# Kernel optimization log

Hardware: AMD Instinct MI355X
Metric: run time of the kernel (lower is better)

The kernel has to match this reference:

```python
import jax, jax.numpy as jnp
import numpy as np

NUM_RANGES = 256
DOPPLER = 64
EMBED = 16
MAX_ELE = 37
MAX_AZI = 107
K_PER_RANGE = 512
IN_DIM = DOPPLER + 2 * EMBED  # 96


def setup_inputs() -> dict:
    key = jax.random.key(0)
    ks = jax.random.split(key, 12)
    N = NUM_RANGES * K_PER_RANGE
    s = 1.0 / np.sqrt(IN_DIM)  # torch Linear default init scale
    return {
        "power_vals": jax.random.normal(ks[0], (N, DOPPLER), dtype=jnp.float32),
        "ele_indices": jax.random.randint(ks[1], (N,), 0, MAX_ELE, dtype=jnp.int32),
        "range_indices": jax.random.randint(ks[2], (N,), 0, NUM_RANGES, dtype=jnp.int32),
        "azi_indices": jax.random.randint(ks[3], (N,), 0, MAX_AZI, dtype=jnp.int32),
        "ele_table": jax.random.normal(ks[4], (MAX_ELE, EMBED), dtype=jnp.float32),
        "azi_table": jax.random.normal(ks[5], (MAX_AZI, EMBED), dtype=jnp.float32),
        "Wq": jax.random.uniform(ks[6], (DOPPLER, IN_DIM), jnp.float32, -s, s),
        "bq": jax.random.uniform(ks[7], (DOPPLER,), jnp.float32, -s, s),
        "Wk": jax.random.uniform(ks[8], (DOPPLER, IN_DIM), jnp.float32, -s, s),
        "bk": jax.random.uniform(ks[9], (DOPPLER,), jnp.float32, -s, s),
        "Wv": jax.random.uniform(ks[10], (DOPPLER, IN_DIM), jnp.float32, -s, s),
        "bv": jax.random.uniform(ks[11], (DOPPLER,), jnp.float32, -s, s),
    }


def reference(power_vals, ele_indices, range_indices, azi_indices,
              ele_table, azi_table, Wq, bq, Wk, bk, Wv, bv):
    Kp = power_vals.shape[0] // NUM_RANGES
    # embedding gather + concat: [R, K, D + 2E]
    ele_e = ele_table[ele_indices.reshape(NUM_RANGES, Kp)]
    azi_e = azi_table[azi_indices.reshape(NUM_RANGES, Kp)]
    pv = power_vals.reshape(NUM_RANGES, Kp, DOPPLER)
    x = jnp.concatenate([pv, ele_e, azi_e], axis=-1)
    # QKV projections (torch Linear: x @ W.T + b)
    Q = jnp.einsum('rkf,df->rkd', x, Wq) + bq
    Kt = jnp.einsum('rkf,df->rkd', x, Wk) + bk
    V = jnp.einsum('rkf,df->rkd', x, Wv) + bv
    scores = jnp.einsum('rqd,rkd->rqk', Q, Kt) / jnp.sqrt(jnp.float32(DOPPLER))
    attn = jax.nn.softmax(scores, axis=-1)
    attended = jnp.einsum('rqk,rkd->rqd', attn, V)
    attended_sum = attended.sum(axis=-1)  # [R, K]
    return attended_sum.reshape(-1)
```

## Files before the change

### kernel.cpp

```cpp
#include <hip/hip_runtime.h>


#define SCALE 0.18033688011112042f

typedef __bf16 bf16;
typedef bf16 v4bf __attribute__((ext_vector_type(4)));
typedef bf16 v8bf __attribute__((ext_vector_type(8)));
typedef float v4f __attribute__((ext_vector_type(4)));

__device__ __forceinline__ v8bf pk8(float4 a, float4 b) {
    v8bf r;
    r[0] = (bf16)a.x; r[1] = (bf16)a.y; r[2] = (bf16)a.z; r[3] = (bf16)a.w;
    r[4] = (bf16)b.x; r[5] = (bf16)b.y; r[6] = (bf16)b.z; r[7] = (bf16)b.w;
    return r;
}
__device__ __forceinline__ float d4(float4 a, v4f w) {
    return a.x * w[0] + a.y * w[1] + a.z * w[2] + a.w * w[3];
}

__global__ __launch_bounds__(1024, 4)
void sda_kernel(const float* __restrict__ power,
                const int*   __restrict__ ele_i,
                const int*   __restrict__ azi_i,
                const float* __restrict__ ele_t,
                const float* __restrict__ azi_t,
                const float* __restrict__ Wq, const float* __restrict__ bq,
                const float* __restrict__ Wk, const float* __restrict__ bk,
                const float* __restrict__ Wv, const float* __restrict__ bv,
                float* __restrict__ out)
{
    extern __shared__ char smem[];
    char*  Kb   = smem;
    float* vsum = (float*)(smem + 65536);
    float* wvs  = (float*)(smem + 67584);

    const int tid  = threadIdx.x;
    const int wave = tid >> 6;
    const int lane = tid & 63;
    const int l15  = lane & 15;
    const int quad = lane >> 4;
    const int rowbase = blockIdx.x * 512 + wave * 32;

    if (tid < 96) {
        float s = 0.f;
#pragma unroll 8
        for (int r = 0; r < 64; r++) s += Wv[r * 96 + tid];
        wvs[tid] = s;
    } else if (tid == 96) {
        float s = 0.f;
#pragma unroll
        for (int d = 0; d < 64; d++) s += bv[d];
        wvs[96] = s;
    }
    __syncthreads();

    v4f w0 = *(const v4f*)(wvs + quad * 8);
    v4f w1 = *(const v4f*)(wvs + quad * 8 + 4);
    v4f w2 = *(const v4f*)(wvs + 32 + quad * 8);
    v4f w3 = *(const v4f*)(wvs + 32 + quad * 8 + 4);
    v4f w4 = *(const v4f*)(wvs + 64 + quad * 8);
    v4f w5 = *(const v4f*)(wvs + 64 + quad * 8 + 4);
    const float bvs = wvs[96];

    v8bf xa[2][3];
#pragma unroll
    for (int mt = 0; mt < 2; mt++) {
        int row = rowbase + mt * 16 + l15;
        const float* pr = power + (size_t)row * 64;
        float4 a0 = *(const float4*)(pr + quad * 8);
        float4 a1 = *(const float4*)(pr + quad * 8 + 4);
        float4 a2 = *(const float4*)(pr + 32 + quad * 8);
        float4 a3 = *(const float4*)(pr + 32 + quad * 8 + 4);
        int ie = ele_i[row];
        int ia = azi_i[row];
        const float* tb = (quad < 2) ? (ele_t + ie * 16 + quad * 8)
                                     : (azi_t + ia * 16 + (quad - 2) * 8);
        float4 a4 = *(const float4*)tb;
        float4 a5 = *(const float4*)(tb + 4);
        xa[mt][0] = pk8(a0, a1);
        xa[mt][1] = pk8(a2, a3);
        xa[mt][2] = pk8(a4, a5);
        float d = d4(a0, w0) + d4(a1, w1) + d4(a2, w2) + d4(a3, w3) + d4(a4, w4) + d4(a5, w5);
        d += __shfl_xor(d, 16);
        d += __shfl_xor(d, 32);
        if (quad == 0) vsum[wave * 32 + mt * 16 + l15] = d + bvs;
    }

    char* Sw = Kb + wave * 4096;
#pragma unroll
    for (int mtd = 0; mtd < 4; mtd++) {
        v8bf wq3[3];
#pragma unroll
        for (int kt = 0; kt < 3; kt++) {
            const float* p = Wq + (mtd * 16 + l15) * 96 + kt * 32 + quad * 8;
            wq3[kt] = pk8(*(const float4*)p, *(const float4*)(p + 4));
        }
        float4 bq4 = *(const float4*)(bq + mtd * 16 + quad * 4);
#pragma unroll
        for (int ntr = 0; ntr < 2; ntr++) {
            v4f acc = {0.f, 0.f, 0.f, 0.f};
#pragma unroll
            for (int kt = 0; kt < 3; kt++)
                acc = __builtin_amdgcn_mfma_f32_16x16x32_bf16(wq3[kt], xa[ntr][kt], acc, 0, 0, 0);
            int row = ntr * 16 + l15;
            v4bf o;
            o[0] = (bf16)((acc[0] + bq4.x) * SCALE);
            o[1] = (bf16)((acc[1] + bq4.y) * SCALE);
            o[2] = (bf16)((acc[2] + bq4.z) * SCALE);
            o[3] = (bf16)((acc[3] + bq4.w) * SCALE);
            *(v4bf*)(Sw + row * 128 +
                     ((((mtd * 2 + (quad >> 1)) ^ (row & 7)) << 4) | ((quad & 1) << 3))) = o;
        }
    }
    v8bf qf[2][2];
#pragma unroll
    for (int nt = 0; nt < 2; nt++)
#pragma unroll
        for (int kt = 0; kt < 2; kt++)
            qf[nt][kt] = *(const v8bf*)(Sw + (nt * 16 + l15) * 128 +
                                        (((kt * 4 + quad) ^ (l15 & 7)) << 4));

#pragma unroll
    for (int mtd = 0; mtd < 4; mtd++) {
        v8bf wk3[3];
#pragma unroll
        for (int kt = 0; kt < 3; kt++) {
            const float* p = Wk + (mtd * 16 + l15) * 96 + kt * 32 + quad * 8;
            wk3[kt] = pk8(*(const float4*)p, *(const float4*)(p + 4));
        }
        float4 bk4 = *(const float4*)(bk + mtd * 16 + quad * 4);
#pragma unroll
        for (int ntr = 0; ntr < 2; ntr++) {
            v4f acc = {0.f, 0.f, 0.f, 0.f};
#pragma unroll
            for (int kt = 0; kt < 3; kt++)
                acc = __builtin_amdgcn_mfma_f32_16x16x32_bf16(wk3[kt], xa[ntr][kt], acc, 0, 0, 0);
            int keyb = wave * 32 + ntr * 16 + l15;
            v4bf o;
            o[0] = (bf16)(acc[0] + bk4.x);
            o[1] = (bf16)(acc[1] + bk4.y);
            o[2] = (bf16)(acc[2] + bk4.z);
            o[3] = (bf16)(acc[3] + bk4.w);
            *(v4bf*)(Kb + keyb * 128 +
                     ((((mtd * 2 + (quad >> 1)) ^ (keyb & 7)) << 4) | ((quad & 1) << 3))) = o;
        }
    }
    __syncthreads();

    float osum[2] = {0.f, 0.f};
    float lsum[2] = {0.f, 0.f};
#pragma unroll 2
    for (int t = 0; t < 16; t++) {
        v8bf kf[2][2];
#pragma unroll
        for (int mtk = 0; mtk < 2; mtk++)
#pragma unroll
            for (int kt = 0; kt < 2; kt++) {
                int key = t * 32 + mtk * 16 + l15;
                kf[mtk][kt] = *(const v8bf*)(Kb + key * 128 + (((kt * 4 + quad) ^ (key & 7)) << 4));
            }
        v4f vs[2];
#pragma unroll
        for (int mtk = 0; mtk < 2; mtk++)
            vs[mtk] = *(const v4f*)(vsum + t * 32 + mtk * 16 + quad * 4);
#pragma unroll
        for (int mtk = 0; mtk < 2; mtk++) {
#pragma unroll
            for (int nt = 0; nt < 2; nt++) {
                v4f acc = {0.f, 0.f, 0.f, 0.f};
                acc = __builtin_amdgcn_mfma_f32_16x16x32_bf16(kf[mtk][0], qf[nt][0], acc, 0, 0, 0);
                acc = __builtin_amdgcn_mfma_f32_16x16x32_bf16(kf[mtk][1], qf[nt][1], acc, 0, 0, 0);
                float p0 = __builtin_amdgcn_exp2f(acc[0]);
                float p1 = __builtin_amdgcn_exp2f(acc[1]);
                float p2 = __builtin_amdgcn_exp2f(acc[2]);
                float p3 = __builtin_amdgcn_exp2f(acc[3]);
                lsum[nt] += (p0 + p1) + (p2 + p3);
                osum[nt] += ((p0 * vs[mtk][0] + p1 * vs[mtk][1]) +
                             (p2 * vs[mtk][2] + p3 * vs[mtk][3]));
            }
        }
    }

#pragma unroll
    for (int nt = 0; nt < 2; nt++) {
        float lv = lsum[nt];
        lv += __shfl_xor(lv, 16);
        lv += __shfl_xor(lv, 32);
        float ov = osum[nt];
        ov += __shfl_xor(ov, 16);
        ov += __shfl_xor(ov, 32);
        if (quad == 0) out[rowbase + nt * 16 + l15] = ov / lv;
    }
}

extern "C" void kernel_launch(void* const* d_in, const int* in_sizes, int n_in,
                              void* d_out, int out_size, void* d_ws, size_t ws_size,
                              hipStream_t stream) {
    const float* power = (const float*)d_in[0];
    const int*   ele_i = (const int*)d_in[1];
    const int*   azi_i = (const int*)d_in[3];
    const float* ele_t = (const float*)d_in[4];
    const float* azi_t = (const float*)d_in[5];
    const float* Wq = (const float*)d_in[6];
    const float* bq = (const float*)d_in[7];
    const float* Wk = (const float*)d_in[8];
    const float* bk = (const float*)d_in[9];
    const float* Wv = (const float*)d_in[10];
    const float* bv = (const float*)d_in[11];
    float* out = (float*)d_out;

    const int lds_bytes = 65536 + 2048 + 512;
    (void)hipFuncSetAttribute(reinterpret_cast<const void*>(sda_kernel),
                              hipFuncAttributeMaxDynamicSharedMemorySize, lds_bytes);
    sda_kernel<<<256, 1024, lds_bytes, stream>>>(power, ele_i, azi_i, ele_t, azi_t,
                                                 Wq, bq, Wk, bk, Wv, bv, out);
}
```

Before: 130.1 us.

## Split each range's queries across two blocks and parallelize the Wv column-sum

The grid doubles to 512 blocks, with two blocks per range. Each block computes all 512 keys and the V-row sums, but only half of the queries, so every wave handles 16 query rows instead of 32. This is meant to fill more CUs on a 256-CU part, at the cost of computing K and the V-sums twice per range. The Wv column-sum becomes a two-stage parallel reduction through LDS, and the bias sum becomes a wave shuffle added at output time. Launch bounds change to request 8 waves per EU.

Result: slower. 190.9 us (+46.8%).

```diff
diff --git a/kernel.cpp b/kernel.cpp
--- a/kernel.cpp
+++ b/kernel.cpp
@@ -18,7 +18,7 @@
     return a.x * w[0] + a.y * w[1] + a.z * w[2] + a.w * w[3];
 }
 
-__global__ __launch_bounds__(1024, 4)
+__global__ __launch_bounds__(1024, 8)
 void sda_kernel(const float* __restrict__ power,
                 const int*   __restrict__ ele_i,
                 const int*   __restrict__ azi_i,
@@ -33,24 +33,36 @@
     char*  Kb   = smem;
     float* vsum = (float*)(smem + 65536);
     float* wvs  = (float*)(smem + 67584);
+    float* wvp  = (float*)Kb;
 
     const int tid  = threadIdx.x;
     const int wave = tid >> 6;
     const int lane = tid & 63;
     const int l15  = lane & 15;
     const int quad = lane >> 4;
-    const int rowbase = blockIdx.x * 512 + wave * 32;
-
+    const int range = blockIdx.x >> 1;
+    const int half  = blockIdx.x & 1;
+    const int krow0 = range * 512 + wave * 32;
+    const int qrow0 = range * 512 + half * 256 + wave * 16;
+
+    float bvs = bv[lane];
+#pragma unroll
+    for (int d = 1; d < 64; d <<= 1) bvs += __shfl_xor(bvs, d);
+
+    if (tid < 768) {
+        int grp = tid / 96, col = tid - grp * 96;
+        const float* p = Wv + grp * 8 * 96 + col;
+        float s = 0.f;
+#pragma unroll
+        for (int r = 0; r < 8; r++) s += p[r * 96];
+        wvp[grp * 96 + col] = s;
+    }
+    __syncthreads();
     if (tid < 96) {
         float s = 0.f;
-#pragma unroll 8
-        for (int r = 0; r < 64; r++) s += Wv[r * 96 + tid];
+#pragma unroll
+        for (int g = 0; g < 8; g++) s += wvp[g * 96 + tid];
         wvs[tid] = s;
-    } else if (tid == 96) {
-        float s = 0.f;
-#pragma unroll
-        for (int d = 0; d < 64; d++) s += bv[d];
-        wvs[96] = s;
     }
     __syncthreads();
 
@@ -60,12 +72,11 @@
     v4f w3 = *(const v4f*)(wvs + 32 + quad * 8 + 4);
     v4f w4 = *(const v4f*)(wvs + 64 + quad * 8);
     v4f w5 = *(const v4f*)(wvs + 64 + quad * 8 + 4);
-    const float bvs = wvs[96];
 
     v8bf xa[2][3];
 #pragma unroll
     for (int mt = 0; mt < 2; mt++) {
-        int row = rowbase + mt * 16 + l15;
+        int row = krow0 + mt * 16 + l15;
         const float* pr = power + (size_t)row * 64;
         float4 a0 = *(const float4*)(pr + quad * 8);
         float4 a1 = *(const float4*)(pr + quad * 8 + 4);
@@ -80,45 +91,56 @@
         xa[mt][0] = pk8(a0, a1);
         xa[mt][1] = pk8(a2, a3);
         xa[mt][2] = pk8(a4, a5);
-        float d = d4(a0, w0) + d4(a1, w1) + d4(a2, w2) + d4(a3, w3) + d4(a4, w4) + d4(a5, w5);
-        d += __shfl_xor(d, 16);
-        d += __shfl_xor(d, 32);
-        if (quad == 0) vsum[wave * 32 + mt * 16 + l15] = d + bvs;
-    }
-
-    char* Sw = Kb + wave * 4096;
-#pragma unroll
-    for (int mtd = 0; mtd < 4; mtd++) {
-        v8bf wq3[3];
-#pragma unroll
-        for (int kt = 0; kt < 3; kt++) {
-            const float* p = Wq + (mtd * 16 + l15) * 96 + kt * 32 + quad * 8;
-            wq3[kt] = pk8(*(const float4*)p, *(const float4*)(p + 4));
-        }
-        float4 bq4 = *(const float4*)(bq + mtd * 16 + quad * 4);
-#pragma unroll
-        for (int ntr = 0; ntr < 2; ntr++) {
+        float dd = d4(a0, w0) + d4(a1, w1) + d4(a2, w2) + d4(a3, w3) + d4(a4, w4) + d4(a5, w5);
+        dd += __shfl_xor(dd, 16);
+        dd += __shfl_xor(dd, 32);
+        if (quad == 0) vsum[wave * 32 + mt * 16 + l15] = dd;
+    }
+
+    v8bf qf[2];
+    {
+        v8bf xq[3];
+        {
+            int row = qrow0 + l15;
+            const float* pr = power + (size_t)row * 64;
+            float4 a0 = *(const float4*)(pr + quad * 8);
+            float4 a1 = *(const float4*)(pr + quad * 8 + 4);
+            float4 a2 = *(const float4*)(pr + 32 + quad * 8);
+            float4 a3 = *(const float4*)(pr + 32 + quad * 8 + 4);
+            int ie = ele_i[row];
+            int ia = azi_i[row];
+            const float* tb = (quad < 2) ? (ele_t + ie * 16 + quad * 8)
+                                         : (azi_t + ia * 16 + (quad - 2) * 8);
+            xq[0] = pk8(a0, a1);
+            xq[1] = pk8(a2, a3);
+            xq[2] = pk8(*(const float4*)tb, *(const float4*)(tb + 4));
+        }
+        char* Sw = Kb + wave * 4096;
+#pragma unroll
+        for (int mtd = 0; mtd < 4; mtd++) {
+            v8bf wq3[3];
+#pragma unroll
+            for (int kt = 0; kt < 3; kt++) {
+                const float* p = Wq + (mtd * 16 + l15) * 96 + kt * 32 + quad * 8;
+                wq3[kt] = pk8(*(const float4*)p, *(const float4*)(p + 4));
+            }
+            float4 bq4 = *(const float4*)(bq + mtd * 16 + quad * 4);
             v4f acc = {0.f, 0.f, 0.f, 0.f};
 #pragma unroll
             for (int kt = 0; kt < 3; kt++)
-                acc = __builtin_amdgcn_mfma_f32_16x16x32_bf16(wq3[kt], xa[ntr][kt], acc, 0, 0, 0);
-            int row = ntr * 16 + l15;
+                acc = __builtin_amdgcn_mfma_f32_16x16x32_bf16(wq3[kt], xq[kt], acc, 0, 0, 0);
             v4bf o;
             o[0] = (bf16)((acc[0] + bq4.x) * SCALE);
             o[1] = (bf16)((acc[1] + bq4.y) * SCALE);
             o[2] = (bf16)((acc[2] + bq4.z) * SCALE);
             o[3] = (bf16)((acc[3] + bq4.w) * SCALE);
-            *(v4bf*)(Sw + row * 128 +
-                     ((((mtd * 2 + (quad >> 1)) ^ (row & 7)) << 4) | ((quad & 1) << 3))) = o;
-        }
-    }
-    v8bf qf[2][2];
-#pragma unroll
-    for (int nt = 0; nt < 2; nt++)
+            *(v4bf*)(Sw + l15 * 128 +
+                     ((((mtd * 2 + (quad >> 1)) ^ (l15 & 7)) << 4) | ((quad & 1) << 3))) = o;
+        }
 #pragma unroll
         for (int kt = 0; kt < 2; kt++)
-            qf[nt][kt] = *(const v8bf*)(Sw + (nt * 16 + l15) * 128 +
-                                        (((kt * 4 + quad) ^ (l15 & 7)) << 4));
+            qf[kt] = *(const v8bf*)(Sw + l15 * 128 + (((kt * 4 + quad) ^ (l15 & 7)) << 4));
+    }
 
 #pragma unroll
     for (int mtd = 0; mtd < 4; mtd++) {
@@ -147,8 +169,7 @@
     }
     __syncthreads();
 
-    float osum[2] = {0.f, 0.f};
-    float lsum[2] = {0.f, 0.f};
+    float osum = 0.f, lsum = 0.f;
 #pragma unroll 2
     for (int t = 0; t < 16; t++) {
         v8bf kf[2][2];
@@ -165,32 +186,26 @@
             vs[mtk] = *(const v4f*)(vsum + t * 32 + mtk * 16 + quad * 4);
 #pragma unroll
         for (int mtk = 0; mtk < 2; mtk++) {
-#pragma unroll
-            for (int nt = 0; nt < 2; nt++) {
-                v4f acc = {0.f, 0.f, 0.f, 0.f};
-                acc = __builtin_amdgcn_mfma_f32_16x16x32_bf16(kf[mtk][0], qf[nt][0], acc, 0, 0, 0);
-                acc = __builtin_amdgcn_mfma_f32_16x16x32_bf16(kf[mtk][1], qf[nt][1], acc, 0, 0, 0);
-                float p0 = __builtin_amdgcn_exp2f(acc[0]);
-                float p1 = __builtin_amdgcn_exp2f(acc[1]);
-                float p2 = __builtin_amdgcn_exp2f(acc[2]);
-                float p3 = __builtin_amdgcn_exp2f(acc[3]);
-                lsum[nt] += (p0 + p1) + (p2 + p3);
-                osum[nt] += ((p0 * vs[mtk][0] + p1 * vs[mtk][1]) +
-                             (p2 * vs[mtk][2] + p3 * vs[mtk][3]));
-            }
-        }
-    }
-
-#pragma unroll
-    for (int nt = 0; nt < 2; nt++) {
-        float lv = lsum[nt];
-        lv += __shfl_xor(lv, 16);
-        lv += __shfl_xor(lv, 32);
-        float ov = osum[nt];
-        ov += __shfl_xor(ov, 16);
-        ov += __shfl_xor(ov, 32);
-        if (quad == 0) out[rowbase + nt * 16 + l15] = ov / lv;
-    }
+            v4f acc = {0.f, 0.f, 0.f, 0.f};
+            acc = __builtin_amdgcn_mfma_f32_16x16x32_bf16(kf[mtk][0], qf[0], acc, 0, 0, 0);
+            acc = __builtin_amdgcn_mfma_f32_16x16x32_bf16(kf[mtk][1], qf[1], acc, 0, 0, 0);
+            float p0 = __builtin_amdgcn_exp2f(acc[0]);
+            float p1 = __builtin_amdgcn_exp2f(acc[1]);
+            float p2 = __builtin_amdgcn_exp2f(acc[2]);
+            float p3 = __builtin_amdgcn_exp2f(acc[3]);
+            lsum += (p0 + p1) + (p2 + p3);
+            osum += ((p0 * vs[mtk][0] + p1 * vs[mtk][1]) +
+                     (p2 * vs[mtk][2] + p3 * vs[mtk][3]));
+        }
+    }
+
+    float lv = lsum;
+    lv += __shfl_xor(lv, 16);
+    lv += __shfl_xor(lv, 32);
+    float ov = osum;
+    ov += __shfl_xor(ov, 16);
+    ov += __shfl_xor(ov, 32);
+    if (quad == 0) out[qrow0 + l15] = ov / lv + bvs;
 }
 
 extern "C" void kernel_launch(void* const* d_in, const int* in_sizes, int n_in,
@@ -212,6 +227,6 @@
     const int lds_bytes = 65536 + 2048 + 512;
     (void)hipFuncSetAttribute(reinterpret_cast<const void*>(sda_kernel),
                               hipFuncAttributeMaxDynamicSharedMemorySize, lds_bytes);
-    sda_kernel<<<256, 1024, lds_bytes, stream>>>(power, ele_i, azi_i, ele_t, azi_t,
+    sda_kernel<<<512, 1024, lds_bytes, stream>>>(power, ele_i, azi_i, ele_t, azi_t,
                                                  Wq, bq, Wk, bk, Wv, bv, out);
 }
```
